# Kernel optimization log

Measured on AMD Instinct MI355X. Metric: run time of the kernel, lower is better.

## Reference

```python
import jax, jax.numpy as jnp
import numpy as np

SCALE_FACTOR = 2  # init kwarg
KERNEL = 1        # kernel=1 -> no Gaussian inpainting of empty cells
EPS = 1e-6


def token2map_agg(x, loc_orig, idx_agg, H, W):
    """Scatter-average aggregated tokens onto a dense [B,C,H,W] map.

    Faithful to token2map_agg_sparse with weight=None, kernel=1:
      each original position i gets feature x[idx_agg[i]] with weight 1,
      scattered to the grid cell of loc_orig[i]; per-cell average with
      denominator (count + 1e-6).
    """
    B, N, C = x.shape
    N0 = loc_orig.shape[1]
    lo = jnp.clip(loc_orig, -1.0, 1.0)
    wh = jnp.array([W, H], dtype=lo.dtype)
    # normalized [-1,1] -> pixel coords, round-half-even like torch.round
    px = jnp.round(0.5 * (lo + 1.0) * wh - 0.5).astype(jnp.int32)
    ix = jnp.clip(px[..., 0], 0, W - 1)
    iy = jnp.clip(px[..., 1], 0, H - 1)
    seg = (iy * W + ix + jnp.arange(B, dtype=jnp.int32)[:, None] * (H * W)).reshape(-1)  # [B*N0]
    # gather token feature for each original position: [B, N0, C]
    feats = jnp.take_along_axis(x, idx_agg[..., None].astype(jnp.int32), axis=1)
    # scatter features and counts together in one segment_sum
    src = jnp.concatenate([feats, jnp.ones_like(feats[..., :1])], axis=-1).reshape(B * N0, C + 1)
    agg = jax.ops.segment_sum(src, seg, num_segments=B * H * W)  # [B*H*W, C+1]
    out = agg[:, :C] / (agg[:, C:] + EPS)
    return out.reshape(B, H, W, C).transpose(0, 3, 1, 2)  # [B,C,H,W]


def setup_inputs() -> dict:
    key = jax.random.key(0)
    k1, k2, k3, k4 = jax.random.split(key, 4)
    B, N, C = 8, 1024, 128
    N0 = 16384  # 128*128 original grid positions
    x = jax.random.normal(k1, (B, N, C), dtype=jnp.float32)
    loc = jax.random.uniform(k2, (B, N, 2), dtype=jnp.float32, minval=-1.0, maxval=1.0)
    loc_orig = jax.random.uniform(k3, (B, N0, 2), dtype=jnp.float32, minval=-1.0, maxval=1.0)
    idx_agg = jax.random.randint(k4, (B, N0), 0, N, dtype=jnp.int32)
    return {"x": x, "loc": loc, "loc_orig": loc_orig, "idx_agg": idx_agg,
            "map_h": 128, "map_w": 128}


def reference(x, loc, loc_orig, idx_agg, map_h, map_w):
    B, N, C = x.shape
    N0 = idx_agg.shape[1]
    scale_orig = (N0 // N) ** 0.5  # static python value
    if SCALE_FACTOR <= scale_orig:
        h, w = int(map_h * SCALE_FACTOR), int(map_w * SCALE_FACTOR)
        out = token2map_agg(x, loc_orig, idx_agg, h, w)
    else:
        h, w = int(map_h * scale_orig), int(map_w * scale_orig)
        out = token2map_agg(x, loc_orig, idx_agg, h, w)
        h, w = int(map_h * SCALE_FACTOR), int(map_w * SCALE_FACTOR)
        out = jax.image.resize(out, (B, C, h, w), method="bilinear")
    return out
```

## Files before the change

### kernel.cpp

```cpp
#include <hip/hip_runtime.h>

constexpr int B  = 8;
constexpr int N  = 1024;
constexpr int C  = 128;
constexpr int N0 = 16384;
constexpr int HH = 256;
constexpr int WW = 256;
constexpr int HW = HH * WW;
constexpr int NPTS = B * N0;

constexpr int CPG  = 64;
constexpr int GPB  = HW / CPG;
constexpr int NGRP = B * GPB;
constexpr int CAP  = 96;

__device__ __forceinline__ int cell_of(float lx, float ly) {
    lx = fminf(fmaxf(lx, -1.0f), 1.0f);
    ly = fminf(fmaxf(ly, -1.0f), 1.0f);
    float pxf = rintf(0.5f * (lx + 1.0f) * 256.0f - 0.5f);
    float pyf = rintf(0.5f * (ly + 1.0f) * 256.0f - 0.5f);
    int ix = (int)pxf; ix = ix < 0 ? 0 : (ix > WW - 1 ? WW - 1 : ix);
    int iy = (int)pyf; iy = iy < 0 ? 0 : (iy > HH - 1 ? HH - 1 : iy);
    return iy * WW + ix;
}

__global__ void bucket_kernel(const float* __restrict__ loc_orig,
                              const int* __restrict__ idx_agg,
                              int* __restrict__ cursor,
                              int* __restrict__ bucket) {
    int p = blockIdx.x * blockDim.x + threadIdx.x;
    if (p >= NPTS) return;
    float2 l = ((const float2*)loc_orig)[p];
    int b = p >> 14;
    int cell = cell_of(l.x, l.y);
    int g = b * GPB + (cell >> 6);
    int pos = atomicAdd(cursor + g, 1);
    if (pos < CAP) bucket[g * CAP + pos] = ((cell & 63) << 10) | idx_agg[p];
}

__global__ __launch_bounds__(256) void gather_kernel(
        const float* __restrict__ x,
        const int* __restrict__ cursor,
        const int* __restrict__ bucket,
        float* __restrict__ out) {
    __shared__ float acc[CPG][C + 1];
    __shared__ int   recs[CAP];
    __shared__ float scale[CPG];

    int gid   = blockIdx.x;
    int b     = gid >> 10;
    int cell0 = (gid & 1023) * CPG;
    int tid   = threadIdx.x;
    int wave  = tid >> 6, lane = tid & 63;

    for (int i = tid; i < CPG * (C + 1); i += 256) ((float*)acc)[i] = 0.0f;

    int cnt = cursor[gid];
    cnt = cnt > CAP ? CAP : cnt;
    if (tid < cnt) recs[tid] = bucket[gid * CAP + tid];
    __syncthreads();

    for (int j = wave; j < cnt; j += 4) {
        int e = recs[j];
        int local = e >> 10;
        int tok   = e & 1023;
        float2 v = ((const float2*)(x + (size_t)(b * N + tok) * C))[lane];
        atomicAdd(&acc[local][lane * 2],     v.x);
        atomicAdd(&acc[local][lane * 2 + 1], v.y);
    }
    __syncthreads();

    if (tid < CPG) {
        int n = 0;
        for (int j = 0; j < cnt; ++j) n += ((recs[j] >> 10) == tid);
        scale[tid] = 1.0f / ((float)n + 1e-6f);
    }
    __syncthreads();

    float* obase = out + (size_t)b * C * HW + cell0;
    int i4 = (tid & 15) * 4;
    int cb = tid >> 4;
    #pragma unroll
    for (int it = 0; it < 8; ++it) {
        int c = cb + 16 * it;
        float4 v;
        v.x = acc[i4 + 0][c] * scale[i4 + 0];
        v.y = acc[i4 + 1][c] * scale[i4 + 1];
        v.z = acc[i4 + 2][c] * scale[i4 + 2];
        v.w = acc[i4 + 3][c] * scale[i4 + 3];
        ((float4*)(obase + (size_t)c * HW))[tid & 15] = v;
    }
}

extern "C" void kernel_launch(void* const* d_in, const int* in_sizes, int n_in,
                              void* d_out, int out_size, void* d_ws, size_t ws_size,
                              hipStream_t stream) {
    const float* x        = (const float*)d_in[0];
    const float* loc_orig = (const float*)d_in[2];
    const int*   idx_agg  = (const int*)d_in[3];
    float* out = (float*)d_out;

    int* cursor = (int*)d_ws;
    int* bucket = cursor + NGRP;

    hipMemsetAsync(cursor, 0, NGRP * sizeof(int), stream);
    bucket_kernel<<<(NPTS + 255) / 256, 256, 0, stream>>>(loc_orig, idx_agg, cursor, bucket);
    gather_kernel<<<NGRP, 256, 0, stream>>>(x, cursor, bucket, out);
}
```

Measured before the change: 361.0 us.

## Double cells per group and transpose LDS accumulator to channel-major layout

```diff
diff --git a/kernel.cpp b/kernel.cpp
--- a/kernel.cpp
+++ b/kernel.cpp
@@ -9,10 +9,14 @@
 constexpr int HW = HH * WW;
 constexpr int NPTS = B * N0;
 
-constexpr int CPG  = 64;
+constexpr int CPG  = 128;
 constexpr int GPB  = HW / CPG;
 constexpr int NGRP = B * GPB;
 constexpr int CAP  = 96;
+
+constexpr int SROW = CPG + 4;
+constexpr int ACC_WORDS = C * SROW;
+constexpr int LDS_BYTES = (ACC_WORDS + CPG + CAP) * 4;
 
 __device__ __forceinline__ int cell_of(float lx, float ly) {
     lx = fminf(fmaxf(lx, -1.0f), 1.0f);
@@ -33,9 +37,9 @@
     float2 l = ((const float2*)loc_orig)[p];
     int b = p >> 14;
     int cell = cell_of(l.x, l.y);
-    int g = b * GPB + (cell >> 6);
+    int g = b * GPB + (cell >> 7);
     int pos = atomicAdd(cursor + g, 1);
-    if (pos < CAP) bucket[g * CAP + pos] = ((cell & 63) << 10) | idx_agg[p];
+    if (pos < CAP) bucket[g * CAP + pos] = ((cell & 127) << 10) | idx_agg[p];
 }
 
 __global__ __launch_bounds__(256) void gather_kernel(
@@ -43,17 +47,20 @@
         const int* __restrict__ cursor,
         const int* __restrict__ bucket,
         float* __restrict__ out) {
-    __shared__ float acc[CPG][C + 1];
-    __shared__ int   recs[CAP];
-    __shared__ float scale[CPG];
+    extern __shared__ float smem[];
+    float* acc  = smem;
+    float* cntf = smem + ACC_WORDS;
+    int*   recs = (int*)(cntf + CPG);
 
     int gid   = blockIdx.x;
-    int b     = gid >> 10;
-    int cell0 = (gid & 1023) * CPG;
+    int b     = gid >> 9;
+    int cell0 = (gid & 511) * CPG;
     int tid   = threadIdx.x;
     int wave  = tid >> 6, lane = tid & 63;
 
-    for (int i = tid; i < CPG * (C + 1); i += 256) ((float*)acc)[i] = 0.0f;
+    float4 z4 = make_float4(0.f, 0.f, 0.f, 0.f);
+    for (int i = tid; i < ACC_WORDS / 4; i += 256) ((float4*)acc)[i] = z4;
+    if (tid < CPG) cntf[tid] = 0.0f;
 
     int cnt = cursor[gid];
     cnt = cnt > CAP ? CAP : cnt;
@@ -65,30 +72,27 @@
         int local = e >> 10;
         int tok   = e & 1023;
         float2 v = ((const float2*)(x + (size_t)(b * N + tok) * C))[lane];
-        atomicAdd(&acc[local][lane * 2],     v.x);
-        atomicAdd(&acc[local][lane * 2 + 1], v.y);
+        atomicAdd(&acc[(2 * lane)     * SROW + local], v.x);
+        atomicAdd(&acc[(2 * lane + 1) * SROW + local], v.y);
+        if (lane == 0) atomicAdd(&cntf[local], 1.0f);
     }
     __syncthreads();
-
-    if (tid < CPG) {
-        int n = 0;
-        for (int j = 0; j < cnt; ++j) n += ((recs[j] >> 10) == tid);
-        scale[tid] = 1.0f / ((float)n + 1e-6f);
-    }
+    if (tid < CPG) cntf[tid] = 1.0f / (cntf[tid] + 1e-6f);
     __syncthreads();
 
+    int sub   = tid & 31;
+    int cpick = tid >> 5;
+    float s0 = cntf[4 * sub + 0];
+    float s1 = cntf[4 * sub + 1];
+    float s2 = cntf[4 * sub + 2];
+    float s3 = cntf[4 * sub + 3];
     float* obase = out + (size_t)b * C * HW + cell0;
-    int i4 = (tid & 15) * 4;
-    int cb = tid >> 4;
     #pragma unroll
-    for (int it = 0; it < 8; ++it) {
-        int c = cb + 16 * it;
-        float4 v;
-        v.x = acc[i4 + 0][c] * scale[i4 + 0];
-        v.y = acc[i4 + 1][c] * scale[i4 + 1];
-        v.z = acc[i4 + 2][c] * scale[i4 + 2];
-        v.w = acc[i4 + 3][c] * scale[i4 + 3];
-        ((float4*)(obase + (size_t)c * HW))[tid & 15] = v;
+    for (int it = 0; it < 16; ++it) {
+        int c = it * 8 + cpick;
+        float4 v = *(const float4*)&acc[c * SROW + 4 * sub];
+        v.x *= s0; v.y *= s1; v.z *= s2; v.w *= s3;
+        ((float4*)(obase + (size_t)c * HW))[sub] = v;
     }
 }
 
@@ -105,5 +109,5 @@
 
     hipMemsetAsync(cursor, 0, NGRP * sizeof(int), stream);
     bucket_kernel<<<(NPTS + 255) / 256, 256, 0, stream>>>(loc_orig, idx_agg, cursor, bucket);
-    gather_kernel<<<NGRP, 256, 0, stream>>>(x, cursor, bucket, out);
+    gather_kernel<<<NGRP, 256, LDS_BYTES, stream>>>(x, cursor, bucket, out);
 }
```

Result: no change. 360.6 us (-0.1%).

## Restructure scatter-average into per-channel strip kernel over transposed features

Applied to the files above, without the earlier changes.

```diff
diff --git a/kernel.cpp b/kernel.cpp
--- a/kernel.cpp
+++ b/kernel.cpp
@@ -12,7 +12,11 @@
 constexpr int CPG  = 64;
 constexpr int GPB  = HW / CPG;
 constexpr int NGRP = B * GPB;
-constexpr int CAP  = 96;
+constexpr int CAP  = 128;
+
+constexpr int STRIP = 4096;
+constexpr int SPB   = HW / STRIP;
+constexpr int GPS   = STRIP / CPG;
 
 __device__ __forceinline__ int cell_of(float lx, float ly) {
     lx = fminf(fmaxf(lx, -1.0f), 1.0f);
@@ -22,6 +26,31 @@
     int ix = (int)pxf; ix = ix < 0 ? 0 : (ix > WW - 1 ? WW - 1 : ix);
     int iy = (int)pyf; iy = iy < 0 ? 0 : (iy > HH - 1 ? HH - 1 : iy);
     return iy * WW + ix;
+}
+
+__global__ __launch_bounds__(256) void transpose_kernel(const float* __restrict__ x,
+                                                        float* __restrict__ xT) {
+    __shared__ float tile[64][C + 1];
+    int blk  = blockIdx.x;
+    int b    = blk >> 4;
+    int tok0 = (blk & 15) * 64;
+    int tid  = threadIdx.x;
+
+    for (int it = 0; it < 8; ++it) {
+        int f  = it * 256 + tid;
+        int tl = f >> 5;
+        int c4 = (f & 31) * 4;
+        float4 v = *(const float4*)(x + ((size_t)(b * N + tok0 + tl) * C + c4));
+        tile[tl][c4 + 0] = v.x; tile[tl][c4 + 1] = v.y;
+        tile[tl][c4 + 2] = v.z; tile[tl][c4 + 3] = v.w;
+    }
+    __syncthreads();
+    for (int it = 0; it < 32; ++it) {
+        int f  = it * 256 + tid;
+        int c  = f >> 6;
+        int tl = f & 63;
+        xT[(size_t)(b * C + c) * N + tok0 + tl] = tile[tl][c];
+    }
 }
 
 __global__ void bucket_kernel(const float* __restrict__ loc_orig,
@@ -35,60 +64,55 @@
     int cell = cell_of(l.x, l.y);
     int g = b * GPB + (cell >> 6);
     int pos = atomicAdd(cursor + g, 1);
-    if (pos < CAP) bucket[g * CAP + pos] = ((cell & 63) << 10) | idx_agg[p];
+    if (pos < CAP) bucket[g * CAP + pos] = (cell << 10) | idx_agg[p];
 }
 
-__global__ __launch_bounds__(256) void gather_kernel(
-        const float* __restrict__ x,
+__global__ __launch_bounds__(256) void strip_kernel(
+        const float* __restrict__ xT,
         const int* __restrict__ cursor,
         const int* __restrict__ bucket,
         float* __restrict__ out) {
-    __shared__ float acc[CPG][C + 1];
-    __shared__ int   recs[CAP];
-    __shared__ float scale[CPG];
+    __shared__ float acc[STRIP];
+    __shared__ float cnt[STRIP];
+    __shared__ float xc[N];
+    int gid = blockIdx.x;
+    int s   = gid & (SPB - 1);
+    int c   = (gid >> 4) & (C - 1);
+    int b   = gid >> 11;
+    int tid = threadIdx.x;
 
-    int gid   = blockIdx.x;
-    int b     = gid >> 10;
-    int cell0 = (gid & 1023) * CPG;
-    int tid   = threadIdx.x;
-    int wave  = tid >> 6, lane = tid & 63;
-
-    for (int i = tid; i < CPG * (C + 1); i += 256) ((float*)acc)[i] = 0.0f;
-
-    int cnt = cursor[gid];
-    cnt = cnt > CAP ? CAP : cnt;
-    if (tid < cnt) recs[tid] = bucket[gid * CAP + tid];
+    float4 z4 = make_float4(0.f, 0.f, 0.f, 0.f);
+    for (int i = tid; i < STRIP / 4; i += 256) {
+        ((float4*)acc)[i] = z4;
+        ((float4*)cnt)[i] = z4;
+    }
+    const float4* xrow = (const float4*)(xT + (size_t)(b * C + c) * N);
+    if (tid < N / 4) ((float4*)xc)[tid] = xrow[tid];
     __syncthreads();
 
-    for (int j = wave; j < cnt; j += 4) {
-        int e = recs[j];
-        int local = e >> 10;
-        int tok   = e & 1023;
-        float2 v = ((const float2*)(x + (size_t)(b * N + tok) * C))[lane];
-        atomicAdd(&acc[local][lane * 2],     v.x);
-        atomicAdd(&acc[local][lane * 2 + 1], v.y);
+    int grp = tid >> 2, j0 = tid & 3;
+    int gg  = b * GPB + s * GPS + grp;
+    int cn  = cursor[gg]; cn = cn > CAP ? CAP : cn;
+    for (int j = j0; j < cn; j += 4) {
+        int rec   = bucket[gg * CAP + j];
+        int local = (rec >> 10) & (STRIP - 1);
+        int tok   = rec & 1023;
+        atomicAdd(&acc[local], xc[tok]);
+        atomicAdd(&cnt[local], 1.0f);
     }
     __syncthreads();
 
-    if (tid < CPG) {
-        int n = 0;
-        for (int j = 0; j < cnt; ++j) n += ((recs[j] >> 10) == tid);
-        scale[tid] = 1.0f / ((float)n + 1e-6f);
-    }
-    __syncthreads();
-
-    float* obase = out + (size_t)b * C * HW + cell0;
-    int i4 = (tid & 15) * 4;
-    int cb = tid >> 4;
+    float* obase = out + (size_t)(b * C + c) * HW + s * STRIP;
     #pragma unroll
-    for (int it = 0; it < 8; ++it) {
-        int c = cb + 16 * it;
-        float4 v;
-        v.x = acc[i4 + 0][c] * scale[i4 + 0];
-        v.y = acc[i4 + 1][c] * scale[i4 + 1];
-        v.z = acc[i4 + 2][c] * scale[i4 + 2];
-        v.w = acc[i4 + 3][c] * scale[i4 + 3];
-        ((float4*)(obase + (size_t)c * HW))[tid & 15] = v;
+    for (int i = 0; i < 4; ++i) {
+        int i4 = i * 256 + tid;
+        float4 a = ((float4*)acc)[i4];
+        float4 n = ((float4*)cnt)[i4];
+        a.x /= (n.x + 1e-6f);
+        a.y /= (n.y + 1e-6f);
+        a.z /= (n.z + 1e-6f);
+        a.w /= (n.w + 1e-6f);
+        ((float4*)obase)[i4] = a;
     }
 }
 
@@ -100,10 +124,12 @@
     const int*   idx_agg  = (const int*)d_in[3];
     float* out = (float*)d_out;
 
-    int* cursor = (int*)d_ws;
-    int* bucket = cursor + NGRP;
+    float* xT     = (float*)d_ws;
+    int*   cursor = (int*)(xT + (size_t)B * C * N);
+    int*   bucket = cursor + NGRP;
 
     hipMemsetAsync(cursor, 0, NGRP * sizeof(int), stream);
+    transpose_kernel<<<B * (N / 64), 256, 0, stream>>>(x, xT);
     bucket_kernel<<<(NPTS + 255) / 256, 256, 0, stream>>>(loc_orig, idx_agg, cursor, bucket);
-    gather_kernel<<<NGRP, 256, 0, stream>>>(x, cursor, bucket, out);
+    strip_kernel<<<B * C * SPB, 256, 0, stream>>>(xT, cursor, bucket, out);
 }
```

Result: slower. 440.4 us (+22.0%).

## Halve cells per gather block and transpose shared accumulator to channel-major

Applied to the files above, without the earlier changes.

```diff
diff --git a/kernel.cpp b/kernel.cpp
--- a/kernel.cpp
+++ b/kernel.cpp
@@ -9,10 +9,13 @@
 constexpr int HW = HH * WW;
 constexpr int NPTS = B * N0;
 
-constexpr int CPG  = 64;
+constexpr int CPG  = 32;
 constexpr int GPB  = HW / CPG;
 constexpr int NGRP = B * GPB;
 constexpr int CAP  = 96;
+
+constexpr int ROW  = CPG + 4;
+constexpr int ACC_WORDS = C * ROW;
 
 __device__ __forceinline__ int cell_of(float lx, float ly) {
     lx = fminf(fmaxf(lx, -1.0f), 1.0f);
@@ -33,9 +36,9 @@
     float2 l = ((const float2*)loc_orig)[p];
     int b = p >> 14;
     int cell = cell_of(l.x, l.y);
-    int g = b * GPB + (cell >> 6);
+    int g = b * GPB + (cell >> 5);
     int pos = atomicAdd(cursor + g, 1);
-    if (pos < CAP) bucket[g * CAP + pos] = ((cell & 63) << 10) | idx_agg[p];
+    if (pos < CAP) bucket[g * CAP + pos] = ((cell & 31) << 10) | idx_agg[p];
 }
 
 __global__ __launch_bounds__(256) void gather_kernel(
@@ -43,52 +46,54 @@
         const int* __restrict__ cursor,
         const int* __restrict__ bucket,
         float* __restrict__ out) {
-    __shared__ float acc[CPG][C + 1];
+    __shared__ float acc[ACC_WORDS];
+    __shared__ float scale[CPG];
     __shared__ int   recs[CAP];
-    __shared__ float scale[CPG];
+    __shared__ int   cnt_s;
 
     int gid   = blockIdx.x;
-    int b     = gid >> 10;
-    int cell0 = (gid & 1023) * CPG;
+    int b     = gid >> 11;
+    int cell0 = (gid & 2047) * CPG;
     int tid   = threadIdx.x;
     int wave  = tid >> 6, lane = tid & 63;
 
-    for (int i = tid; i < CPG * (C + 1); i += 256) ((float*)acc)[i] = 0.0f;
+    int my_cnt = (tid == 0) ? cursor[gid] : 0;
+    int my_rec = (tid < CAP) ? bucket[gid * CAP + tid] : 0;
 
-    int cnt = cursor[gid];
-    cnt = cnt > CAP ? CAP : cnt;
-    if (tid < cnt) recs[tid] = bucket[gid * CAP + tid];
+    float4 z4 = make_float4(0.f, 0.f, 0.f, 0.f);
+    for (int i = tid; i < ACC_WORDS / 4; i += 256) ((float4*)acc)[i] = z4;
+    if (tid < CPG) scale[tid] = 0.0f;
+
+    if (tid == 0) cnt_s = my_cnt > CAP ? CAP : my_cnt;
+    if (tid < CAP) recs[tid] = my_rec;
     __syncthreads();
+
+    int cnt = cnt_s;
 
     for (int j = wave; j < cnt; j += 4) {
         int e = recs[j];
         int local = e >> 10;
         int tok   = e & 1023;
         float2 v = ((const float2*)(x + (size_t)(b * N + tok) * C))[lane];
-        atomicAdd(&acc[local][lane * 2],     v.x);
-        atomicAdd(&acc[local][lane * 2 + 1], v.y);
+        atomicAdd(&acc[(2 * lane)     * ROW + local], v.x);
+        atomicAdd(&acc[(2 * lane + 1) * ROW + local], v.y);
+        if (lane == 0) atomicAdd(&scale[local], 1.0f);
     }
     __syncthreads();
-
-    if (tid < CPG) {
-        int n = 0;
-        for (int j = 0; j < cnt; ++j) n += ((recs[j] >> 10) == tid);
-        scale[tid] = 1.0f / ((float)n + 1e-6f);
-    }
+    if (tid < CPG) scale[tid] = 1.0f / (scale[tid] + 1e-6f);
     __syncthreads();
 
+    int i4 = (tid & 7) * 4;
+    int cb = tid >> 3;
+    float s0 = scale[i4 + 0], s1 = scale[i4 + 1];
+    float s2 = scale[i4 + 2], s3 = scale[i4 + 3];
     float* obase = out + (size_t)b * C * HW + cell0;
-    int i4 = (tid & 15) * 4;
-    int cb = tid >> 4;
     #pragma unroll
-    for (int it = 0; it < 8; ++it) {
-        int c = cb + 16 * it;
-        float4 v;
-        v.x = acc[i4 + 0][c] * scale[i4 + 0];
-        v.y = acc[i4 + 1][c] * scale[i4 + 1];
-        v.z = acc[i4 + 2][c] * scale[i4 + 2];
-        v.w = acc[i4 + 3][c] * scale[i4 + 3];
-        ((float4*)(obase + (size_t)c * HW))[tid & 15] = v;
+    for (int it = 0; it < 4; ++it) {
+        int c = it * 32 + cb;
+        float4 v = *(const float4*)&acc[c * ROW + i4];
+        v.x *= s0; v.y *= s1; v.z *= s2; v.w *= s3;
+        *(float4*)(obase + (size_t)c * HW + i4) = v;
     }
 }
 
```

Result: no change. 354.2 us (-1.9%).
